# Kernel tuning notes

Measured on AMD Instinct MI355X. Metric: run time of the kernel, lower is better.

The kernel has to match this reference:

```python
import jax, jax.numpy as jnp
import numpy as np

EMBED_DIM = 1024
ATTN_DIM = 1024


def setup_inputs() -> dict:
    key = jax.random.key(0)
    k1, k2, k3, k4 = jax.random.split(key, 4)
    embedded = jax.random.normal(k1, (4, 2048, EMBED_DIM), dtype=jnp.float32)
    # torch nn.Linear weights are [out_features, in_features]
    s = 1.0 / np.sqrt(EMBED_DIM)
    Wk = jax.random.uniform(k2, (ATTN_DIM, EMBED_DIM), jnp.float32, -s, s)
    Wq = jax.random.uniform(k3, (ATTN_DIM, EMBED_DIM), jnp.float32, -s, s)
    Wv = jax.random.uniform(k4, (ATTN_DIM, EMBED_DIM), jnp.float32, -s, s)
    return {"embedded": embedded, "Wk": Wk, "Wq": Wq, "Wv": Wv}


def reference(embedded, Wk, Wq, Wv):
    # projections: x @ W.T  (torch Linear, no bias)
    k = jnp.einsum("bse,ae->bsa", embedded, Wk)
    q = jnp.einsum("bse,ae->bsa", embedded, Wq)
    v = jnp.einsum("bse,ae->bsa", embedded, Wv)
    scale = 1.0 / jnp.sqrt(jnp.float32(ATTN_DIM))
    attn = jnp.einsum("bqa,bka->bqk", q, k) * scale  # [B, S, S]
    S = attn.shape[1]
    causal = jnp.tril(jnp.ones((S, S), dtype=bool))
    attn = jnp.where(causal[None, :, :], attn, -jnp.inf)
    a = jax.nn.softmax(attn, axis=2)
    out = jnp.einsum("bqk,bka->bqa", a, v)
    return jnp.round(out, 4)
```

## Files before the change

kernel.cpp:

```cpp
#include <hip/hip_runtime.h>
#include <hip/hip_bf16.h>
#include <hip/hip_fp16.h>
#include <stdint.h>

typedef __bf16 bf16_t;
typedef bf16_t bf16x8 __attribute__((ext_vector_type(8)));
typedef bf16_t bf16x4 __attribute__((ext_vector_type(4)));
typedef float f32x4 __attribute__((ext_vector_type(4)));

#define BM 128
#define BN 128
#define BK 32

__device__ __forceinline__ void gload_lds16(const void* g, void* l) {
    __builtin_amdgcn_global_load_lds(
        (const __attribute__((address_space(1))) void*)(uintptr_t)g,
        (__attribute__((address_space(3))) void*)(uintptr_t)l,
        16, 0, 0);
}

template <int EPI>
__device__ __forceinline__ void gemm_body(
    bf16_t* __restrict__ As, bf16_t* __restrict__ Bs,
    const bf16_t* __restrict__ A, long lda,
    const bf16_t* __restrict__ B, long ldb,
    void* __restrict__ Cv, long ldc,
    int k0beg, int k1end, float scale, int m0, int n0,
    float* __restrict__ rs)
{
    const int tid = threadIdx.x;
    const int wid = tid >> 6, lane = tid & 63;
    const int wr = wid >> 1, wc = wid & 1;
    const int hw = lane >> 4, ln = lane & 15;

    const bf16_t *srcA[2], *srcB[2];
#pragma unroll
    for (int i = 0; i < 2; i++) {
        const int c = tid + i * 256;
        const int row = c >> 2;
        const int j = ((c & 3) - (row >> 1)) & 3;
        srcA[i] = A + (size_t)(m0 + row) * lda + j * 8;
        srcB[i] = B + (size_t)(n0 + row) * ldb + j * 8;
    }

    f32x4 acc[4][4] = {};

    for (int k0 = k0beg; k0 < k1end; k0 += BK) {
        gload_lds16(srcA[0] + k0, &As[wid * 512]);
        gload_lds16(srcA[1] + k0, &As[2048 + wid * 512]);
        gload_lds16(srcB[0] + k0, &Bs[wid * 512]);
        gload_lds16(srcB[1] + k0, &Bs[2048 + wid * 512]);
        __syncthreads();

        bf16x8 af[4], bfr[4];
#pragma unroll
        for (int t = 0; t < 4; t++) {
            const int r  = wr * 64 + t * 16 + ln;
            const int rb = wc * 64 + t * 16 + ln;
            af[t]  = *(const bf16x8*)&As[r  * BK + (((hw + (r  >> 1)) & 3) * 8)];
            bfr[t] = *(const bf16x8*)&Bs[rb * BK + (((hw + (rb >> 1)) & 3) * 8)];
        }
#pragma unroll
        for (int ti = 0; ti < 4; ti++)
#pragma unroll
            for (int tj = 0; tj < 4; tj++)
                acc[ti][tj] = __builtin_amdgcn_mfma_f32_16x16x32_bf16(
                    af[ti], bfr[tj], acc[ti][tj], 0, 0, 0);
        __syncthreads();
    }

#pragma unroll
    for (int ti = 0; ti < 4; ti++) {
        const int rbase = m0 + wr * 64 + ti * 16 + hw * 4;
        f32x4 inv4;
        if (EPI == 2) {
            const float4 r4 = *(const float4*)&rs[rbase];
            inv4[0] = 1.0f / r4.x; inv4[1] = 1.0f / r4.y;
            inv4[2] = 1.0f / r4.z; inv4[3] = 1.0f / r4.w;
        }
        float part[4] = {0.f, 0.f, 0.f, 0.f};
#pragma unroll
        for (int tj = 0; tj < 4; tj++) {
            const int col = n0 + wc * 64 + tj * 16 + ln;
            if (EPI == 4) {
                const int bb = rbase >> 11;
                const int s  = rbase & 2047;
                const int d  = col - 2048;
                bf16x4 o;
#pragma unroll
                for (int rg = 0; rg < 4; rg++) o[rg] = (bf16_t)acc[ti][tj][rg];
                *(bf16x4*)&((bf16_t*)Cv)[(size_t)bb * 2097152 + (size_t)d * 2048 + s] = o;
            } else {
#pragma unroll
                for (int rg = 0; rg < 4; rg++) {
                    const size_t idx = (size_t)(rbase + rg) * ldc + col;
                    if (EPI == 2) {
                        ((float*)Cv)[idx] = acc[ti][tj][rg] * inv4[rg];
                    } else {
                        const float e = (col <= rbase + rg)
                                      ? __expf(acc[ti][tj][rg] * scale) : 0.0f;
                        part[rg] += e;
                        ((bf16_t*)Cv)[idx] = (bf16_t)e;
                    }
                }
            }
        }
        if (EPI == 3) {
#pragma unroll
            for (int rg = 0; rg < 4; rg++) {
                float p = part[rg];
                p += __shfl_xor(p, 1, 64);
                p += __shfl_xor(p, 2, 64);
                p += __shfl_xor(p, 4, 64);
                p += __shfl_xor(p, 8, 64);
                if (ln == 0) atomicAdd(&rs[rbase + rg], p);
            }
        }
    }
}

__device__ __forceinline__ void gemm256_body(
    bf16_t* __restrict__ lds,
    const bf16_t* __restrict__ A, long lda,
    const bf16_t* __restrict__ B, long ldb,
    bf16_t* __restrict__ C, long ldc,
    int nt, int m0, int n0)
{
    const int tid = threadIdx.x;
    const int wid = tid >> 6, lane = tid & 63;
    const int wr = wid >> 2, wcn = wid & 3;
    const int hw = lane >> 4, ln = lane & 15;

    const int srow = (wid << 3) + (lane >> 3);
    const int clog = ((lane & 7) - (lane >> 3)) & 7;
    const bf16_t* sA = A + (size_t)(m0 + srow) * lda + clog * 8;
    const bf16_t* sB = B + (size_t)(n0 + srow) * ldb + clog * 8;
    char* ldsc = (char*)lds;
    const int wb = wid << 10;

#define STG_A(bf, q, kt) gload_lds16(sA + (size_t)(q) * 64 * lda + (size_t)(kt) * 64, \
                                     ldsc + (bf) * 65536 + (q) * 8192 + wb)
#define STG_B(bf, q, kt) gload_lds16(sB + (size_t)(q) * 64 * ldb + (size_t)(kt) * 64, \
                                     ldsc + (bf) * 65536 + 32768 + (q) * 8192 + wb)

    const int c0 = ((hw + ln) & 7) << 4;
    const int c1 = ((hw + ln + 4) & 7) << 4;
    const int aR = (wr * 128 + ln) * 128;
    const int bR = 32768 + (wcn * 64 + ln) * 128;

#define RDA(bf, fr, ks) (*(const bf16x8*)(ldsc + (bf) * 65536 + aR + (fr) * 2048 + ((ks) ? c1 : c0)))
#define RDB(bf, fc, ks) (*(const bf16x8*)(ldsc + (bf) * 65536 + bR + (fc) * 2048 + ((ks) ? c1 : c0)))

    f32x4 acc[8][4] = {};

    STG_A(0, 0, 0); STG_A(0, 2, 0); STG_B(0, 0, 0); STG_B(0, 1, 0);
    STG_A(0, 1, 0); STG_A(0, 3, 0); STG_B(0, 2, 0); STG_B(0, 3, 0);
    STG_A(1, 0, 1); STG_A(1, 2, 1); STG_B(1, 0, 1); STG_B(1, 1, 1);
    STG_A(1, 1, 1); STG_A(1, 3, 1);
    asm volatile("s_waitcnt vmcnt(6)" ::: "memory");
    __builtin_amdgcn_s_barrier();

    for (int t = 0; t < nt; ++t) {
        const int bc = t & 1, bn = bc ^ 1;
        const int kt1 = (t + 1) & (nt - 1);
        const int kt2 = (t + 2) & (nt - 1);
        bf16x8 af[4][2], bl[2][2], bh[2][2];

#pragma unroll
        for (int fr = 0; fr < 4; ++fr) {
            af[fr][0] = RDA(bc, fr, 0);
            af[fr][1] = RDA(bc, fr, 1);
        }
#pragma unroll
        for (int fc = 0; fc < 2; ++fc) {
            bl[fc][0] = RDB(bc, fc, 0);
            bl[fc][1] = RDB(bc, fc, 1);
        }
        STG_B(bn, 2, kt1); STG_B(bn, 3, kt1);
        __builtin_amdgcn_s_barrier();
        asm volatile("s_waitcnt lgkmcnt(0)" ::: "memory");
        __builtin_amdgcn_sched_barrier(0);
        __builtin_amdgcn_s_setprio(1);
#pragma unroll
        for (int fr = 0; fr < 4; ++fr)
#pragma unroll
            for (int fc = 0; fc < 2; ++fc)
#pragma unroll
                for (int ks = 0; ks < 2; ++ks)
                    acc[fr][fc] = __builtin_amdgcn_mfma_f32_16x16x32_bf16(
                        af[fr][ks], bl[fc][ks], acc[fr][fc], 0, 0, 0);
        __builtin_amdgcn_s_setprio(0);
        __builtin_amdgcn_s_barrier();

#pragma unroll
        for (int fc = 0; fc < 2; ++fc) {
            bh[fc][0] = RDB(bc, fc + 2, 0);
            bh[fc][1] = RDB(bc, fc + 2, 1);
        }
        STG_A(bc, 0, kt2); STG_A(bc, 2, kt2);
        __builtin_amdgcn_s_barrier();
        asm volatile("s_waitcnt lgkmcnt(0)" ::: "memory");
        __builtin_amdgcn_sched_barrier(0);
        __builtin_amdgcn_s_setprio(1);
#pragma unroll
        for (int fr = 0; fr < 4; ++fr)
#pragma unroll
            for (int fc = 0; fc < 2; ++fc)
#pragma unroll
                for (int ks = 0; ks < 2; ++ks)
                    acc[fr][fc + 2] = __builtin_amdgcn_mfma_f32_16x16x32_bf16(
                        af[fr][ks], bh[fc][ks], acc[fr][fc + 2], 0, 0, 0);
        __builtin_amdgcn_s_setprio(0);
        __builtin_amdgcn_s_barrier();

#pragma unroll
        for (int fr = 0; fr < 4; ++fr) {
            af[fr][0] = RDA(bc, fr + 4, 0);
            af[fr][1] = RDA(bc, fr + 4, 1);
        }
        STG_B(bc, 0, kt2); STG_B(bc, 1, kt2);
        __builtin_amdgcn_s_barrier();
        asm volatile("s_waitcnt lgkmcnt(0)" ::: "memory");
        __builtin_amdgcn_sched_barrier(0);
        __builtin_amdgcn_s_setprio(1);
#pragma unroll
        for (int fr = 0; fr < 4; ++fr)
#pragma unroll
            for (int fc = 0; fc < 2; ++fc)
#pragma unroll
                for (int ks = 0; ks < 2; ++ks)
                    acc[fr + 4][fc + 2] = __builtin_amdgcn_mfma_f32_16x16x32_bf16(
                        af[fr][ks], bh[fc][ks], acc[fr + 4][fc + 2], 0, 0, 0);
        __builtin_amdgcn_s_setprio(0);
        __builtin_amdgcn_s_barrier();

        STG_A(bc, 1, kt2); STG_A(bc, 3, kt2);
        __builtin_amdgcn_s_setprio(1);
#pragma unroll
        for (int fr = 0; fr < 4; ++fr)
#pragma unroll
            for (int fc = 0; fc < 2; ++fc)
#pragma unroll
                for (int ks = 0; ks < 2; ++ks)
                    acc[fr + 4][fc] = __builtin_amdgcn_mfma_f32_16x16x32_bf16(
                        af[fr][ks], bl[fc][ks], acc[fr + 4][fc], 0, 0, 0);
        __builtin_amdgcn_s_setprio(0);
        asm volatile("s_waitcnt vmcnt(6)" ::: "memory");
        __builtin_amdgcn_s_barrier();
    }

    asm volatile("s_waitcnt vmcnt(0)" ::: "memory");

#pragma unroll
    for (int fr = 0; fr < 8; ++fr) {
        const int rbase = m0 + wr * 128 + fr * 16 + hw * 4;
#pragma unroll
        for (int fc = 0; fc < 4; ++fc) {
            const int col = n0 + wcn * 64 + fc * 16 + ln;
#pragma unroll
            for (int rg = 0; rg < 4; rg++)
                C[(size_t)(rbase + rg) * ldc + col] = (bf16_t)acc[fr][fc][rg];
        }
    }
#undef STG_A
#undef STG_B
#undef RDA
#undef RDB
}

__global__ __launch_bounds__(512, 2) void gemm1_kq(
    const bf16_t* __restrict__ xb, const bf16_t* __restrict__ Wb,
    bf16_t* __restrict__ QKVb)
{
    __shared__ __align__(16) bf16_t lds[65536];
    const int lin = blockIdx.x;
    const int xcd = lin & 7;
    const int j   = lin >> 3;
    const int mblk = xcd * 4 + (j & 3);
    const int nblk = j >> 2;
    gemm256_body(lds, xb, 1024, Wb, 1024, QKVb, 2048, 16, mblk * 256, nblk * 256);
}

__global__ __launch_bounds__(256) void gemm1_v(
    const bf16_t* __restrict__ xb, const bf16_t* __restrict__ Wb,
    bf16_t* __restrict__ Vt)
{
    __shared__ __align__(16) bf16_t As[BM * BK];
    __shared__ __align__(16) bf16_t Bs[BN * BK];
    const int lin = blockIdx.x;
    const int xcd = lin & 7;
    const int j   = lin >> 3;
    const int mblk = xcd * 8 + (j >> 3);
    const int nblk = j & 7;
    gemm_body<4>(As, Bs, xb, 1024, Wb, 1024, Vt, 2048,
                 0, 1024, 1.0f, mblk * BM, 2048 + nblk * BN, nullptr);
}

__global__ __launch_bounds__(256) void qk_gemm(
    const bf16_t* __restrict__ QKVb, bf16_t* __restrict__ E,
    float* __restrict__ rowsum)
{
    __shared__ __align__(16) bf16_t As[BM * BK];
    __shared__ __align__(16) bf16_t Bs[BN * BK];
    const int b = blockIdx.x & 3;
    int rem = blockIdx.x >> 2;
    int my = 15, nx = 0;
#pragma unroll
    for (int m = 15; m >= 0; --m) {
        if (rem < m + 1) { my = m; nx = rem; break; }
        rem -= m + 1;
    }
    const bf16_t* base = QKVb + (size_t)b * (2048L * 2048);
    gemm_body<3>(As, Bs,
                 base + 1024, 2048,
                 base, 2048,
                 E + (size_t)b * (2048L * 2048), 2048,
                 0, 1024, 0.03125f, my * BM, nx * BN,
                 rowsum + b * 2048);
}

__global__ __launch_bounds__(256) void gemm3_pv(
    const bf16_t* __restrict__ E, const bf16_t* __restrict__ Vt,
    const float* __restrict__ rowsum, float* __restrict__ out)
{
    __shared__ __align__(16) bf16_t As[BM * BK];
    __shared__ __align__(16) bf16_t Bs[BN * BK];
    const int id = blockIdx.x;
    const int strip = 15 - (id >> 5);
    const int nx = (id >> 2) & 7;
    const int b = id & 3;
    const int m0 = strip * BM;
    gemm_body<2>(As, Bs,
                 E + (size_t)b * (2048L * 2048), 2048,
                 Vt + (size_t)b * (1024L * 2048), 2048,
                 out + (size_t)b * (2048L * 1024), 1024,
                 0, m0 + BM, 1.0f, m0, nx * BN,
                 (float*)rowsum + b * 2048);
}

__global__ __launch_bounds__(256) void cast_all(
    const float* __restrict__ x,
    const float* __restrict__ Wk, const float* __restrict__ Wq,
    const float* __restrict__ Wv,
    bf16_t* __restrict__ xb, bf16_t* __restrict__ Wb,
    float* __restrict__ rowsum)
{
    const int blk = blockIdx.x;
    if (blk >= 11264) {
        const size_t i = ((size_t)(blk - 11264) * 256 + threadIdx.x) * 4;
        *(float4*)(rowsum + i) = make_float4(0.f, 0.f, 0.f, 0.f);
        return;
    }
    const float* src;
    bf16_t* dst;
    if (blk < 8192) {
        const size_t i = ((size_t)blk * 256 + threadIdx.x) * 4;
        src = x + i;
        dst = xb + i;
    } else {
        const size_t j = ((size_t)(blk - 8192) * 256 + threadIdx.x) * 4;
        dst = Wb + j;
        if (j < (size_t)1048576)      src = Wk + j;
        else if (j < (size_t)2097152) src = Wq + (j - 1048576);
        else                          src = Wv + (j - 2097152);
    }
    const float4 v = *(const float4*)src;
    bf16x4 o;
    o.x = (bf16_t)v.x; o.y = (bf16_t)v.y; o.z = (bf16_t)v.z; o.w = (bf16_t)v.w;
    *(bf16x4*)dst = o;
}

extern "C" void kernel_launch(void* const* d_in, const int* in_sizes, int n_in,
                              void* d_out, int out_size, void* d_ws, size_t ws_size,
                              hipStream_t stream)
{
    const float* x  = (const float*)d_in[0];
    const float* Wk = (const float*)d_in[1];
    const float* Wq = (const float*)d_in[2];
    const float* Wv = (const float*)d_in[3];
    char* ws = (char*)d_ws;

    bf16_t* QKVb   = (bf16_t*)(ws);
    bf16_t* Vt     = (bf16_t*)(ws + ((size_t)32 << 20));
    bf16_t* xb     = (bf16_t*)(ws + ((size_t)48 << 20));
    bf16_t* Wb     = (bf16_t*)(ws + ((size_t)64 << 20));
    bf16_t* E      = (bf16_t*)(ws + ((size_t)48 << 20));
    float*  rowsum = (float*)(ws + ((size_t)80 << 20));
    float*  out    = (float*)d_out;

    cast_all<<<11272, 256, 0, stream>>>(x, Wk, Wq, Wv, xb, Wb, rowsum);

    gemm1_kq<<<256, 512, 0, stream>>>(xb, Wb, QKVb);

    gemm1_v<<<512, 256, 0, stream>>>(xb, Wb, Vt);

    qk_gemm<<<544, 256, 0, stream>>>(QKVb, E, rowsum);

    gemm3_pv<<<512, 256, 0, stream>>>(E, Vt, rowsum, out);
}
```

Before: 224.9 us.

## Fuse V projection and QK GEMM into one launch; double K-tile depth

Raises BK from 32 to 64 with an 8-chunk XOR-style LDS swizzle, halving barrier count per K loop in the 128x128 GEMM body. Adds a combined kernel that runs the V projection blocks and the causal QK^T blocks in a single grid of 1056 blocks. To do that, E is moved to a separate workspace region so it no longer aliases xb when the workspace is large enough. This removes one launch and the tail gap between two kernels, at the cost of doubled LDS per block, which may lower occupancy.

Result: no change. 224.8 us (-0.1%).

```diff
diff --git a/kernel.cpp b/kernel.cpp
--- a/kernel.cpp
+++ b/kernel.cpp
@@ -10,7 +10,7 @@
 
 #define BM 128
 #define BN 128
-#define BK 32
+#define BK 64
 
 __device__ __forceinline__ void gload_lds16(const void* g, void* l) {
     __builtin_amdgcn_global_load_lds(
@@ -33,39 +33,38 @@
     const int wr = wid >> 1, wc = wid & 1;
     const int hw = lane >> 4, ln = lane & 15;
 
-    const bf16_t *srcA[2], *srcB[2];
-#pragma unroll
-    for (int i = 0; i < 2; i++) {
-        const int c = tid + i * 256;
-        const int row = c >> 2;
-        const int j = ((c & 3) - (row >> 1)) & 3;
-        srcA[i] = A + (size_t)(m0 + row) * lda + j * 8;
-        srcB[i] = B + (size_t)(n0 + row) * ldb + j * 8;
-    }
+    const int row0 = tid >> 3;
+    const int jj = ((tid & 7) - (row0 >> 1)) & 7;
+    const bf16_t* srcA0 = A + (size_t)(m0 + row0) * lda + jj * 8;
+    const bf16_t* srcB0 = B + (size_t)(n0 + row0) * ldb + jj * 8;
 
     f32x4 acc[4][4] = {};
 
     for (int k0 = k0beg; k0 < k1end; k0 += BK) {
-        gload_lds16(srcA[0] + k0, &As[wid * 512]);
-        gload_lds16(srcA[1] + k0, &As[2048 + wid * 512]);
-        gload_lds16(srcB[0] + k0, &Bs[wid * 512]);
-        gload_lds16(srcB[1] + k0, &Bs[2048 + wid * 512]);
+#pragma unroll
+        for (int i = 0; i < 4; i++) {
+            gload_lds16(srcA0 + (size_t)(32 * i) * lda + k0, &As[tid * 8 + i * 2048]);
+            gload_lds16(srcB0 + (size_t)(32 * i) * ldb + k0, &Bs[tid * 8 + i * 2048]);
+        }
         __syncthreads();
 
-        bf16x8 af[4], bfr[4];
-#pragma unroll
-        for (int t = 0; t < 4; t++) {
-            const int r  = wr * 64 + t * 16 + ln;
-            const int rb = wc * 64 + t * 16 + ln;
-            af[t]  = *(const bf16x8*)&As[r  * BK + (((hw + (r  >> 1)) & 3) * 8)];
-            bfr[t] = *(const bf16x8*)&Bs[rb * BK + (((hw + (rb >> 1)) & 3) * 8)];
-        }
-#pragma unroll
-        for (int ti = 0; ti < 4; ti++)
-#pragma unroll
-            for (int tj = 0; tj < 4; tj++)
-                acc[ti][tj] = __builtin_amdgcn_mfma_f32_16x16x32_bf16(
-                    af[ti], bfr[tj], acc[ti][tj], 0, 0, 0);
+#pragma unroll
+        for (int h = 0; h < 2; h++) {
+            bf16x8 af[4], bfr[4];
+#pragma unroll
+            for (int t = 0; t < 4; t++) {
+                const int r  = wr * 64 + t * 16 + ln;
+                const int rb = wc * 64 + t * 16 + ln;
+                af[t]  = *(const bf16x8*)&As[r  * BK + ((((h << 2) + hw) + (r  >> 1)) & 7) * 8];
+                bfr[t] = *(const bf16x8*)&Bs[rb * BK + ((((h << 2) + hw) + (rb >> 1)) & 7) * 8];
+            }
+#pragma unroll
+            for (int ti = 0; ti < 4; ti++)
+#pragma unroll
+                for (int tj = 0; tj < 4; tj++)
+                    acc[ti][tj] = __builtin_amdgcn_mfma_f32_16x16x32_bf16(
+                        af[ti], bfr[tj], acc[ti][tj], 0, 0, 0);
+        }
         __syncthreads();
     }
 
@@ -279,6 +278,42 @@
     const int mblk = xcd * 4 + (j & 3);
     const int nblk = j >> 2;
     gemm256_body(lds, xb, 1024, Wb, 1024, QKVb, 2048, 16, mblk * 256, nblk * 256);
+}
+
+__global__ __launch_bounds__(256) void vqk_fused(
+    const bf16_t* __restrict__ xb, const bf16_t* __restrict__ Wb,
+    bf16_t* __restrict__ Vt,
+    const bf16_t* __restrict__ QKVb, bf16_t* __restrict__ E,
+    float* __restrict__ rowsum)
+{
+    __shared__ __align__(16) bf16_t As[BM * BK];
+    __shared__ __align__(16) bf16_t Bs[BN * BK];
+    const int id = blockIdx.x;
+    if (id < 512) {
+        const int xcd = id & 7;
+        const int j   = id >> 3;
+        const int mblk = xcd * 8 + (j >> 3);
+        const int nblk = j & 7;
+        gemm_body<4>(As, Bs, xb, 1024, Wb, 1024, Vt, 2048,
+                     0, 1024, 1.0f, mblk * BM, 2048 + nblk * BN, nullptr);
+    } else {
+        const int qid = id - 512;
+        const int b = qid & 3;
+        int rem = qid >> 2;
+        int my = 15, nx = 0;
+#pragma unroll
+        for (int m = 15; m >= 0; --m) {
+            if (rem < m + 1) { my = m; nx = rem; break; }
+            rem -= m + 1;
+        }
+        const bf16_t* base = QKVb + (size_t)b * (2048L * 2048);
+        gemm_body<3>(As, Bs,
+                     base + 1024, 2048,
+                     base, 2048,
+                     E + (size_t)b * (2048L * 2048), 2048,
+                     0, 1024, 0.03125f, my * BM, nx * BN,
+                     rowsum + b * 2048);
+    }
 }
 
 __global__ __launch_bounds__(256) void gemm1_v(
@@ -380,21 +415,25 @@
     const float* Wv = (const float*)d_in[3];
     char* ws = (char*)d_ws;
 
-    bf16_t* QKVb   = (bf16_t*)(ws);
-    bf16_t* Vt     = (bf16_t*)(ws + ((size_t)32 << 20));
-    bf16_t* xb     = (bf16_t*)(ws + ((size_t)48 << 20));
-    bf16_t* Wb     = (bf16_t*)(ws + ((size_t)64 << 20));
-    bf16_t* E      = (bf16_t*)(ws + ((size_t)48 << 20));
-    float*  rowsum = (float*)(ws + ((size_t)80 << 20));
+    bf16_t* QKVb = (bf16_t*)(ws);
+    bf16_t* Vt   = (bf16_t*)(ws + ((size_t)32 << 20));
+    bf16_t* xb   = (bf16_t*)(ws + ((size_t)48 << 20));
+    bf16_t* Wb   = (bf16_t*)(ws + ((size_t)64 << 20));
+    const bool big = ws_size >= ((size_t)107 << 20);
+    bf16_t* E      = (bf16_t*)(ws + ((size_t)(big ? 72 : 48) << 20));
+    float*  rowsum = (float*)(ws + ((size_t)(big ? 106 : 80) << 20));
     float*  out    = (float*)d_out;
 
     cast_all<<<11272, 256, 0, stream>>>(x, Wk, Wq, Wv, xb, Wb, rowsum);
 
     gemm1_kq<<<256, 512, 0, stream>>>(xb, Wb, QKVb);
 
-    gemm1_v<<<512, 256, 0, stream>>>(xb, Wb, Vt);
-
-    qk_gemm<<<544, 256, 0, stream>>>(QKVb, E, rowsum);
+    if (big) {
+        vqk_fused<<<1056, 256, 0, stream>>>(xb, Wb, Vt, QKVb, E, rowsum);
+    } else {
+        gemm1_v<<<512, 256, 0, stream>>>(xb, Wb, Vt);
+        qk_gemm<<<544, 256, 0, stream>>>(QKVb, E, rowsum);
+    }
 
     gemm3_pv<<<512, 256, 0, stream>>>(E, Vt, rowsum, out);
 }
```
